# Optimization experiments

Measured on AMD Instinct MI355X. Metric: run time of the kernel, lower is better.

The kernel has to match this reference:

```python
import jax, jax.numpy as jnp
import numpy as np

B, C, N = 8, 128, 4096
C2 = C // 2
BN_EPS = 1e-5


def setup_inputs() -> dict:
    key = jax.random.key(0)
    ks = jax.random.split(key, 8)
    s = 1.0 / np.sqrt(C)
    s2 = 1.0 / np.sqrt(C2)
    return {
        "x": jax.random.normal(ks[0], (B, C, N), dtype=jnp.float32),
        "w_qk": jax.random.uniform(ks[1], (C2, C), jnp.float32, -s, s),  # shared q/k weight
        "w_v": jax.random.uniform(ks[2], (C2, C), jnp.float32, -s, s),
        "b_v": jax.random.uniform(ks[3], (C2,), jnp.float32, -s, s),
        "w_x": jax.random.uniform(ks[4], (C2, C), jnp.float32, -s, s),
        "w_t": jax.random.uniform(ks[5], (C2, C2), jnp.float32, -s2, s2),
        "b_t": jax.random.uniform(ks[6], (C2,), jnp.float32, -s2, s2),
        "gamma": jnp.ones((C2,), jnp.float32),
        "beta": jnp.zeros((C2,), jnp.float32),
    }


def reference(x, w_qk, w_v, b_v, w_x, w_t, b_t, gamma, beta):
    # 1x1 convs are per-point linear maps: [B,C,N] -> [B,C2,N]
    x_q = jnp.einsum("oc,bcn->bno", w_qk, x)          # [B, N, C2]
    x_k = jnp.einsum("oc,bcn->bon", w_qk, x)          # [B, C2, N]
    x_v = jnp.einsum("oc,bcn->bon", w_v, x) + b_v[None, :, None]

    energy = jnp.einsum("bno,bom->bnm", x_q, x_k)     # [B, N, N]
    attn = jax.nn.softmax(energy, axis=-1)            # row softmax
    attn = attn / (1e-9 + attn.sum(axis=1, keepdims=True))  # column L1 renorm

    x_r = jnp.einsum("bon,bnm->bom", x_v, attn)       # [B, C2, N]
    x_c = jnp.einsum("oc,bcn->bon", w_x, x)           # [B, C2, N]

    d = x_c - x_r
    t = jnp.einsum("oi,bin->bon", w_t, d) + b_t[None, :, None]
    # BatchNorm1d (training-mode batch stats) over (B, N) per channel
    mean = t.mean(axis=(0, 2), keepdims=True)
    var = t.var(axis=(0, 2), keepdims=True)
    t_hat = (t - mean) * jax.lax.rsqrt(var + BN_EPS)
    x_r2 = jax.nn.relu(gamma[None, :, None] * t_hat + beta[None, :, None])
    return x_c + x_r2
```

## Files before the change

### kernel.cpp

```cpp
#include <hip/hip_runtime.h>

#define B_   8
#define C_   128
#define N_   4096
#define C2_  64

typedef __bf16 bf16x8 __attribute__((ext_vector_type(8)));
typedef float  f32x4  __attribute__((ext_vector_type(4)));

#define MFMA16(a, b, c) __builtin_amdgcn_mfma_f32_16x16x32_bf16((a), (b), (c), 0, 0, 0)

#define QK_SCALE 1.2011224087864498f

static __device__ __forceinline__ unsigned short f2bf(float f) {
    union { __bf16 b; unsigned short u; } cv;
    cv.b = (__bf16)f;
    return cv.u;
}
static __device__ __forceinline__ float bf2f(unsigned short u) {
    union { unsigned int u; float f; } cv;
    cv.u = ((unsigned int)u) << 16;
    return cv.f;
}

struct us4 { unsigned short a, b, c, d; };

static __device__ __forceinline__ void gl_lds16(const unsigned short* g, void* l) {
    __builtin_amdgcn_global_load_lds(
        (const __attribute__((address_space(1))) unsigned int*)g,
        (__attribute__((address_space(3))) unsigned int*)l,
        16, 0, 0);
}

__global__ __launch_bounds__(256) void k1_proj(
    const float* __restrict__ x, const float* __restrict__ w_qk,
    const float* __restrict__ w_v, const float* __restrict__ b_v,
    const float* __restrict__ w_x,
    unsigned short* __restrict__ qk_t, unsigned short* __restrict__ xv_bf,
    float* __restrict__ xc)
{
    __shared__ __align__(16) unsigned short w_lds[192 * 136];
    __shared__ __align__(16) unsigned short x_t[64 * 136];
    const int tid = threadIdx.x;
    const int wave = tid >> 6, lane = tid & 63;
    const int quad = lane >> 4, col = lane & 15;
    const int b = blockIdx.y;
    const int n0 = blockIdx.x * 64;

    const float* wsrc[3] = {w_qk, w_v, w_x};
    #pragma unroll
    for (int mat = 0; mat < 3; ++mat) {
        const float* wm = wsrc[mat];
        #pragma unroll
        for (int it = 0; it < 8; ++it) {
            const int idx = it * 256 + tid;
            const int o = idx >> 5, c = (idx & 31) * 4;
            const float4 v = *(const float4*)(wm + o * C_ + c);
            us4 pk;
            pk.a = f2bf(v.x); pk.b = f2bf(v.y); pk.c = f2bf(v.z); pk.d = f2bf(v.w);
            *(us4*)&w_lds[(mat * 64 + o) * 136 + c] = pk;
        }
    }
    const float* xb = x + (size_t)b * C_ * N_ + n0;
    #pragma unroll
    for (int it = 0; it < 8; ++it) {
        const int idx = it * 256 + tid;
        const int c = idx >> 4, n = (idx & 15) * 4;
        const float4 v = *(const float4*)(xb + (size_t)c * N_ + n);
        x_t[(n + 0) * 136 + c] = f2bf(v.x);
        x_t[(n + 1) * 136 + c] = f2bf(v.y);
        x_t[(n + 2) * 136 + c] = f2bf(v.z);
        x_t[(n + 3) * 136 + c] = f2bf(v.w);
    }
    __syncthreads();

    const int nw = wave * 16;
    bf16x8 bfr[4];
    #pragma unroll
    for (int kt = 0; kt < 4; ++kt)
        bfr[kt] = *(const bf16x8*)&x_t[(nw + col) * 136 + kt * 32 + quad * 8];

    const int n_g = n0 + nw + col;

    #pragma unroll
    for (int ot = 0; ot < 12; ++ot) {
        f32x4 acc = {0.f, 0.f, 0.f, 0.f};
        #pragma unroll
        for (int kt = 0; kt < 4; ++kt) {
            const bf16x8 afr = *(const bf16x8*)&w_lds[(ot * 16 + col) * 136 + kt * 32 + quad * 8];
            acc = MFMA16(afr, bfr[kt], acc);
        }
        if (ot < 4) {
            us4 pk;
            pk.a = f2bf(acc[0] * QK_SCALE); pk.b = f2bf(acc[1] * QK_SCALE);
            pk.c = f2bf(acc[2] * QK_SCALE); pk.d = f2bf(acc[3] * QK_SCALE);
            *(us4*)&qk_t[(size_t)(b * N_ + n_g) * C2_ + ot * 16 + quad * 4] = pk;
        } else if (ot < 8) {
            const float4 bv4 = *(const float4*)(b_v + (ot - 4) * 16 + quad * 4);
            const float* bvp = (const float*)&bv4;
            #pragma unroll
            for (int r = 0; r < 4; ++r)
                xv_bf[(size_t)(b * C2_ + (ot - 4) * 16 + quad * 4 + r) * N_ + n_g]
                    = f2bf(acc[r] + bvp[r]);
        } else {
            #pragma unroll
            for (int r = 0; r < 4; ++r)
                xc[(size_t)(b * C2_ + (ot - 8) * 16 + quad * 4 + r) * N_ + n_g] = acc[r];
        }
    }
}

__global__ __launch_bounds__(256) void k2_rowstats(
    const unsigned short* __restrict__ qk_t, float* __restrict__ part_rs)
{
    __shared__ __align__(16) unsigned char lds_raw[2 * 16384];
    const int tid = threadIdx.x;
    const int wave = tid >> 6, lane = tid & 63;
    const int quad = lane >> 4, col = lane & 15;
    const int b = blockIdx.x & 7;
    const int nblk = (blockIdx.x >> 3) & 31;
    const int mq = blockIdx.x >> 8;
    const int n_base = nblk * 128 + wave * 32;
    const int m_start = mq * 512;
    const unsigned short* qb = qk_t + (size_t)b * N_ * C2_;

    bf16x8 a0[2], a1[2];
    #pragma unroll
    for (int s = 0; s < 2; ++s) {
        const unsigned short* p = qb + (size_t)(n_base + s * 16 + col) * C2_ + quad * 8;
        a0[s] = *(const bf16x8*)p;
        a1[s] = *(const bf16x8*)(p + 32);
    }

    auto stage = [&](int m0, int p) {
        unsigned char* base = lds_raw + p * 16384;
        #pragma unroll
        for (int r = 0; r < 4; ++r) {
            const int idx = r * 256 + tid;
            const int row = idx >> 3, seg = idx & 7;
            gl_lds16(qb + (size_t)(m0 + row) * C2_ + (size_t)(seg ^ (row & 7)) * 8,
                     base + idx * 16);
        }
    };

    float run_s[2][4];
    #pragma unroll
    for (int s = 0; s < 2; ++s)
        #pragma unroll
        for (int r = 0; r < 4; ++r) run_s[s][r] = 0.f;

    stage(m_start, 0);

    for (int c = 0; c < 4; ++c) {
        const int p = c & 1;
        asm volatile("s_waitcnt vmcnt(0)" ::: "memory");
        __builtin_amdgcn_s_barrier();
        asm volatile("" ::: "memory");
        if (c + 1 < 4) stage(m_start + (c + 1) * 128, 1 - p);
        const unsigned short* qt = (const unsigned short*)(lds_raw + p * 16384);
        #pragma unroll
        for (int ms = 0; ms < 8; ++ms) {
            const int row = ms * 16 + col;
            const bf16x8 b0 = *(const bf16x8*)(qt + row * 64 + ((quad ^ (col & 7)) * 8));
            const bf16x8 b1 = *(const bf16x8*)(qt + row * 64 + (((4 + quad) ^ (col & 7)) * 8));
            #pragma unroll
            for (int s = 0; s < 2; ++s) {
                f32x4 acc = {0.f, 0.f, 0.f, 0.f};
                __builtin_amdgcn_s_setprio(1);
                acc = MFMA16(a0[s], b0, acc);
                acc = MFMA16(a1[s], b1, acc);
                __builtin_amdgcn_s_setprio(0);
                #pragma unroll
                for (int r = 0; r < 4; ++r)
                    run_s[s][r] += __builtin_amdgcn_exp2f(acc[r]);
            }
        }
    }

    #pragma unroll
    for (int s = 0; s < 2; ++s)
        #pragma unroll
        for (int r = 0; r < 4; ++r) {
            #pragma unroll
            for (int off = 1; off < 16; off <<= 1)
                run_s[s][r] += __shfl_xor(run_s[s][r], off, 64);
        }
    if (col == 0) {
        #pragma unroll
        for (int s = 0; s < 2; ++s)
            #pragma unroll
            for (int r = 0; r < 4; ++r)
                part_rs[((size_t)(mq * 8 + b) << 12) + n_base + s * 16 + quad * 4 + r]
                    = run_s[s][r];
    }
}

__global__ __launch_bounds__(256) void k2bc(
    const float* __restrict__ part_rs, unsigned short* __restrict__ xv_bf,
    unsigned short* __restrict__ wbf)
{
    __shared__ float wl[64];
    const int tid = threadIdx.x;
    const int b = blockIdx.x & 7;
    const int n0 = (blockIdx.x >> 3) * 64;
    if (tid < 64) {
        float s = 0.f;
        #pragma unroll
        for (int q = 0; q < 8; ++q)
            s += part_rs[((size_t)(q * 8 + b) << 12) + n0 + tid];
        const float w = 1.0f / s;
        wl[tid] = w;
        wbf[b * N_ + n0 + tid] = f2bf(w);
    }
    __syncthreads();
    #pragma unroll
    for (int it = 0; it < 4; ++it) {
        const int idx4 = it * 256 + tid;
        const int o = idx4 >> 4, n4 = (idx4 & 15) * 4;
        unsigned short* p = xv_bf + (size_t)(b * C2_ + o) * N_ + n0 + n4;
        us4 v = *(us4*)p;
        v.a = f2bf(bf2f(v.a) * wl[n4 + 0]);
        v.b = f2bf(bf2f(v.b) * wl[n4 + 1]);
        v.c = f2bf(bf2f(v.c) * wl[n4 + 2]);
        v.d = f2bf(bf2f(v.d) * wl[n4 + 3]);
        *(us4*)p = v;
    }
}

__global__ __launch_bounds__(512, 4) void k3_pv(
    const unsigned short* __restrict__ qk_t, const unsigned short* __restrict__ xv_bf,
    const unsigned short* __restrict__ wbf,
    unsigned short* __restrict__ yb0, unsigned short* __restrict__ yb1,
    float* __restrict__ cspart)
{
    __shared__ __align__(16) unsigned char lds_raw[32768 + 8 * 2560];
    const int tid = threadIdx.x;
    const int wave = tid >> 6, lane = tid & 63;
    const int quad = lane >> 4, col = lane & 15;
    const int nh2 = wave & 1, mh = wave >> 1;
    const int b = blockIdx.x & 7;
    const int m_blk = ((blockIdx.x >> 3) & 31) * 128;
    const int sk = blockIdx.x >> 8;
    const int n_start = sk * 2048;
    const int n_chunks = 32;
    const int m_wave = m_blk + mh * 32;
    const unsigned short* qb = qk_t + (size_t)b * N_ * C2_;
    const unsigned short* vb = xv_bf + (size_t)b * C2_ * N_;
    const unsigned short* wb = wbf + b * N_;
    unsigned short* yp = (sk == 0) ? yb0 : yb1;

    bf16x8 kb0[2], kb1[2];
    #pragma unroll
    for (int g = 0; g < 2; ++g) {
        const unsigned short* p = qb + (size_t)(m_wave + g * 16 + col) * C2_ + quad * 8;
        kb0[g] = *(const bf16x8*)p;
        kb1[g] = *(const bf16x8*)(p + 32);
    }

    unsigned short* stS = (unsigned short*)(lds_raw + 32768 + wave * 2560);

    auto stage = [&](int n0, int p) {
        unsigned char* qbase = lds_raw + p * 8192;
        unsigned char* vbase = lds_raw + 16384 + p * 8192;
        const int row = tid >> 3, seg = tid & 7;
        const int ss = seg ^ (row & 7);
        gl_lds16(qb + (size_t)(n0 + row) * C2_ + (size_t)ss * 8, qbase + tid * 16);
        gl_lds16(vb + (size_t)row * N_ + n0 + ss * 8, vbase + tid * 16);
    };

    f32x4 accY[2][4];
    #pragma unroll
    for (int g = 0; g < 2; ++g)
        #pragma unroll
        for (int os = 0; os < 4; ++os) accY[g][os] = (f32x4){0.f, 0.f, 0.f, 0.f};
    f32x4 csacc[2];
    #pragma unroll
    for (int g = 0; g < 2; ++g) csacc[g] = (f32x4){0.f, 0.f, 0.f, 0.f};

    stage(n_start, 0);
    __syncthreads();

    for (int c = 0; c < n_chunks; ++c) {
        const int n0 = n_start + c * 64;
        const int p = c & 1;
        if (c + 1 < n_chunks) stage(n0 + 64, 1 - p);

        const unsigned short* qt = (const unsigned short*)(lds_raw + p * 8192);
        const unsigned short* vt = (const unsigned short*)(lds_raw + 16384 + p * 8192);

        const bf16x8 wfrag = *(const bf16x8*)(wb + n0 + nh2 * 32 + quad * 8);

        #pragma unroll
        for (int ns = 0; ns < 2; ++ns) {
            const int row = nh2 * 32 + ns * 16 + col;
            const bf16x8 qa0 = *(const bf16x8*)(qt + row * 64 + ((quad ^ (col & 7)) * 8));
            const bf16x8 qa1 = *(const bf16x8*)(qt + row * 64 + (((4 + quad) ^ (col & 7)) * 8));
            #pragma unroll
            for (int g = 0; g < 2; ++g) {
                f32x4 acc = {0.f, 0.f, 0.f, 0.f};
                acc = MFMA16(qa0, kb0[g], acc);
                acc = MFMA16(qa1, kb1[g], acc);
                union { unsigned short us[4]; uint2 u2; } pk;
                #pragma unroll
                for (int r = 0; r < 4; ++r)
                    pk.us[r] = f2bf(__builtin_amdgcn_exp2f(acc[r]));
                *(uint2*)&stS[(g * 16 + col) * 40 + ns * 16 + quad * 4] = pk.u2;
            }
        }

        bf16x8 sB[2];
        #pragma unroll
        for (int g = 0; g < 2; ++g)
            sB[g] = *(const bf16x8*)&stS[(g * 16 + col) * 40 + quad * 8];

        #pragma unroll
        for (int g = 0; g < 2; ++g)
            csacc[g] = MFMA16(wfrag, sB[g], csacc[g]);

        #pragma unroll
        for (int os = 0; os < 4; ++os) {
            const bf16x8 va = *(const bf16x8*)(vt + (os * 16 + col) * 64 +
                                               (((nh2 * 4 + quad) ^ (col & 7)) * 8));
            #pragma unroll
            for (int g = 0; g < 2; ++g)
                accY[g][os] = MFMA16(va, sB[g], accY[g][os]);
        }
        __syncthreads();
    }

    float* cmb = (float*)lds_raw;
    float* csc = (float*)(lds_raw + 32768);
    if (nh2 == 1) {
        #pragma unroll
        for (int g = 0; g < 2; ++g) {
            #pragma unroll
            for (int os = 0; os < 4; ++os)
                #pragma unroll
                for (int r = 0; r < 4; ++r)
                    cmb[((mh * 8 + g * 4 + os) * 4 + r) * 64 + lane] = accY[g][os][r];
            csc[(mh * 2 + g) * 64 + lane] = csacc[g][0];
        }
    }
    __syncthreads();
    if (nh2 == 0) {
        #pragma unroll
        for (int g = 0; g < 2; ++g) {
            const float cs = csacc[g][0] + csc[(mh * 2 + g) * 64 + lane];
            if (lane < 16)
                cspart[((size_t)sk * 8 + b) * N_ + m_wave + g * 16 + lane] = cs;
            #pragma unroll
            for (int os = 0; os < 4; ++os)
                #pragma unroll
                for (int r = 0; r < 4; ++r) {
                    const float v = accY[g][os][r] +
                        cmb[((mh * 8 + g * 4 + os) * 4 + r) * 64 + lane];
                    yp[(size_t)(b * C2_ + os * 16 + quad * 4 + r) * N_ + m_wave + g * 16 + col]
                        = f2bf(v);
                }
        }
    }
}

__global__ __launch_bounds__(256) void k4_t(
    const float* __restrict__ xc, const unsigned short* __restrict__ y0,
    const unsigned short* __restrict__ y1,
    const float* __restrict__ cspart, const float* __restrict__ w_t,
    const float* __restrict__ b_t, float* __restrict__ t_buf,
    float* __restrict__ part_bn)
{
    __shared__ __align__(16) unsigned short wlds[64 * 72];
    __shared__ __align__(16) unsigned short d_t[64 * 72];
    __shared__ float cinv[64];
    const int tid = threadIdx.x;
    const int wave = tid >> 6, lane = tid & 63;
    const int quad = lane >> 4, col = lane & 15;
    const int b = blockIdx.y;
    const int n0 = blockIdx.x * 64;
    const size_t base = (size_t)b * C2_ * N_;

    #pragma unroll
    for (int it = 0; it < 4; ++it) {
        const int idx4 = it * 256 + tid;
        const int o = idx4 >> 4, i4 = (idx4 & 15) * 4;
        const float4 v = *(const float4*)(w_t + o * 64 + i4);
        us4 pk;
        pk.a = f2bf(v.x); pk.b = f2bf(v.y); pk.c = f2bf(v.z); pk.d = f2bf(v.w);
        *(us4*)&wlds[o * 72 + i4] = pk;
    }
    if (tid < 64) {
        const int n = n0 + tid;
        const float cs = cspart[(size_t)b * N_ + n] + cspart[(size_t)(8 + b) * N_ + n];
        cinv[tid] = 1.0f / (1e-9f + cs);
    }
    __syncthreads();

    #pragma unroll
    for (int it = 0; it < 4; ++it) {
        const int idx4 = it * 256 + tid;
        const int i = idx4 >> 4, n4 = (idx4 & 15) * 4;
        const size_t g = base + (size_t)i * N_ + n0 + n4;
        const float4 c4 = *(const float4*)(xc + g);
        const us4 u0 = *(const us4*)(y0 + g);
        const us4 u1 = *(const us4*)(y1 + g);
        d_t[(n4 + 0) * 72 + i] = f2bf(c4.x - (bf2f(u0.a) + bf2f(u1.a)) * cinv[n4 + 0]);
        d_t[(n4 + 1) * 72 + i] = f2bf(c4.y - (bf2f(u0.b) + bf2f(u1.b)) * cinv[n4 + 1]);
        d_t[(n4 + 2) * 72 + i] = f2bf(c4.z - (bf2f(u0.c) + bf2f(u1.c)) * cinv[n4 + 2]);
        d_t[(n4 + 3) * 72 + i] = f2bf(c4.w - (bf2f(u0.d) + bf2f(u1.d)) * cinv[n4 + 3]);
    }
    __syncthreads();

    const int ow = wave * 16;
    bf16x8 afr[2];
    #pragma unroll
    for (int kt = 0; kt < 2; ++kt)
        afr[kt] = *(const bf16x8*)&wlds[(ow + col) * 72 + kt * 32 + quad * 8];
    const float4 bt4 = *(const float4*)(b_t + ow + quad * 4);
    const float* btp = (const float*)&bt4;

    float s[4] = {0.f, 0.f, 0.f, 0.f}, q2[4] = {0.f, 0.f, 0.f, 0.f};
    #pragma unroll
    for (int ns = 0; ns < 4; ++ns) {
        f32x4 acc = {0.f, 0.f, 0.f, 0.f};
        #pragma unroll
        for (int kt = 0; kt < 2; ++kt) {
            const bf16x8 bfr = *(const bf16x8*)&d_t[(ns * 16 + col) * 72 + kt * 32 + quad * 8];
            acc = MFMA16(afr[kt], bfr, acc);
        }
        #pragma unroll
        for (int r = 0; r < 4; ++r) {
            const float t = acc[r] + btp[r];
            t_buf[base + (size_t)(ow + quad * 4 + r) * N_ + n0 + ns * 16 + col] = t;
            s[r] += t;
            q2[r] += t * t;
        }
    }
    #pragma unroll
    for (int r = 0; r < 4; ++r) {
        #pragma unroll
        for (int off = 1; off < 16; off <<= 1) {
            s[r]  += __shfl_xor(s[r],  off, 64);
            q2[r] += __shfl_xor(q2[r], off, 64);
        }
    }
    if (col == 0) {
        const int blk = blockIdx.x * 8 + b;
        #pragma unroll
        for (int r = 0; r < 4; ++r) {
            part_bn[(size_t)(ow + quad * 4 + r) * 512 + blk]      = s[r];
            part_bn[(size_t)(64 + ow + quad * 4 + r) * 512 + blk] = q2[r];
        }
    }
}

__global__ __launch_bounds__(256) void k5r(
    const float* __restrict__ part_bn, float* __restrict__ bn)
{
    const int c = blockIdx.x;
    const int tid = threadIdx.x, wave = tid >> 6, lane = tid & 63;
    float s = 0.f;
    for (int j = tid; j < 512; j += 256) s += part_bn[(size_t)c * 512 + j];
    #pragma unroll
    for (int off = 1; off < 64; off <<= 1) s += __shfl_xor(s, off, 64);
    __shared__ float red[4];
    if (lane == 0) red[wave] = s;
    __syncthreads();
    if (tid == 0) bn[c] = red[0] + red[1] + red[2] + red[3];
}

__global__ __launch_bounds__(256) void k6_out(
    const float* __restrict__ xc, const float* __restrict__ t_buf,
    const float* __restrict__ bn, const float* __restrict__ gamma,
    const float* __restrict__ beta, float* __restrict__ out)
{
    const int idx = blockIdx.x * 256 + threadIdx.x;
    const int o = (idx >> 10) & 63;
    const float invC = 1.0f / (float)(B_ * N_);
    const float mean = bn[o] * invC;
    const float var  = bn[64 + o] * invC - mean * mean;
    const float sc = gamma[o] * rsqrtf(var + 1e-5f);
    const float sh = beta[o] - mean * sc;
    const float4 t4 = ((const float4*)t_buf)[idx];
    const float4 c4 = ((const float4*)xc)[idx];
    float4 r;
    r.x = c4.x + fmaxf(0.f, sc * t4.x + sh);
    r.y = c4.y + fmaxf(0.f, sc * t4.y + sh);
    r.z = c4.z + fmaxf(0.f, sc * t4.z + sh);
    r.w = c4.w + fmaxf(0.f, sc * t4.w + sh);
    ((float4*)out)[idx] = r;
}

extern "C" void kernel_launch(void* const* d_in, const int* in_sizes, int n_in,
                              void* d_out, int out_size, void* d_ws, size_t ws_size,
                              hipStream_t stream) {
    const float* x     = (const float*)d_in[0];
    const float* w_qk  = (const float*)d_in[1];
    const float* w_v   = (const float*)d_in[2];
    const float* b_v   = (const float*)d_in[3];
    const float* w_x   = (const float*)d_in[4];
    const float* w_t   = (const float*)d_in[5];
    const float* b_t   = (const float*)d_in[6];
    const float* gamma = (const float*)d_in[7];
    const float* beta  = (const float*)d_in[8];
    float* out = (float*)d_out;

    char* ws = (char*)d_ws;
    unsigned short* qk_t  = (unsigned short*)ws;
    unsigned short* xv_bf = (unsigned short*)(ws + (4  << 20));
    float* xc      = (float*)(ws + (8  << 20));
    unsigned short* yb0 = (unsigned short*)(ws + (16 << 20));
    unsigned short* yb1 = (unsigned short*)(ws + (20 << 20));
    float* t_buf   = (float*)(ws + (24 << 20));
    float* part_rs = (float*)(ws + (32 << 20));
    float* cspart  = (float*)(ws + (32 << 20));
    unsigned short* wbf = (unsigned short*)(ws + (33 << 20));
    float* part_bn = (float*)(ws + (33 << 20) + (64 << 10));
    float* bn      = (float*)(ws + (33 << 20) + (320 << 10));

    hipLaunchKernelGGL(k1_proj,     dim3(64, 8),  256, 0, stream,
                       x, w_qk, w_v, b_v, w_x, qk_t, xv_bf, xc);
    hipLaunchKernelGGL(k2_rowstats, dim3(2048),   256, 0, stream, qk_t, part_rs);
    hipLaunchKernelGGL(k2bc,        dim3(512),    256, 0, stream, part_rs, xv_bf, wbf);
    hipLaunchKernelGGL(k3_pv,       dim3(512),    512, 0, stream,
                       qk_t, xv_bf, wbf, yb0, yb1, cspart);
    hipLaunchKernelGGL(k4_t,        dim3(64, 8),  256, 0, stream,
                       xc, yb0, yb1, cspart, w_t, b_t, t_buf, part_bn);
    hipLaunchKernelGGL(k5r,         dim3(128),    256, 0, stream, part_bn, bn);
    hipLaunchKernelGGL(k6_out,      dim3(2048),   256, 0, stream, xc, t_buf, bn, gamma, beta, out);
}
```

Measured before the change: 165.1 us.

## Software-pipeline PV loop: compute exp(S) of next chunk while MMA-ing previous

Restructures the k3_pv main loop into a skewed software pipeline. The QK/exp phase for chunk c is issued before the PV and column-sum MFMAs for chunk c-1, and the S tiles are double-buffered in LDS. V fragments and weights are register-prefetched one iteration ahead. The aim is to overlap the exp/transcendental work with the MFMA work and drop a sync stall, at the cost of more LDS, more registers, and lowering launch_bounds occupancy from 4 to 3.

```diff
diff --git a/kernel.cpp b/kernel.cpp
--- a/kernel.cpp
+++ b/kernel.cpp
@@ -227,13 +227,13 @@
     }
 }
 
-__global__ __launch_bounds__(512, 4) void k3_pv(
+__global__ __launch_bounds__(512, 3) void k3_pv(
     const unsigned short* __restrict__ qk_t, const unsigned short* __restrict__ xv_bf,
     const unsigned short* __restrict__ wbf,
     unsigned short* __restrict__ yb0, unsigned short* __restrict__ yb1,
     float* __restrict__ cspart)
 {
-    __shared__ __align__(16) unsigned char lds_raw[32768 + 8 * 2560];
+    __shared__ __align__(16) unsigned char lds_raw[32768 + 8 * 5120];
     const int tid = threadIdx.x;
     const int wave = tid >> 6, lane = tid & 63;
     const int quad = lane >> 4, col = lane & 15;
@@ -257,7 +257,7 @@
         kb1[g] = *(const bf16x8*)(p + 32);
     }
 
-    unsigned short* stS = (unsigned short*)(lds_raw + 32768 + wave * 2560);
+    unsigned short* stSb = (unsigned short*)(lds_raw + 32768 + wave * 5120);
 
     auto stage = [&](int n0, int p) {
         unsigned char* qbase = lds_raw + p * 8192;
@@ -268,28 +268,9 @@
         gl_lds16(vb + (size_t)row * N_ + n0 + ss * 8, vbase + tid * 16);
     };
 
-    f32x4 accY[2][4];
-    #pragma unroll
-    for (int g = 0; g < 2; ++g)
-        #pragma unroll
-        for (int os = 0; os < 4; ++os) accY[g][os] = (f32x4){0.f, 0.f, 0.f, 0.f};
-    f32x4 csacc[2];
-    #pragma unroll
-    for (int g = 0; g < 2; ++g) csacc[g] = (f32x4){0.f, 0.f, 0.f, 0.f};
-
-    stage(n_start, 0);
-    __syncthreads();
-
-    for (int c = 0; c < n_chunks; ++c) {
-        const int n0 = n_start + c * 64;
-        const int p = c & 1;
-        if (c + 1 < n_chunks) stage(n0 + 64, 1 - p);
-
+    auto ephase = [&](int p) {
         const unsigned short* qt = (const unsigned short*)(lds_raw + p * 8192);
-        const unsigned short* vt = (const unsigned short*)(lds_raw + 16384 + p * 8192);
-
-        const bf16x8 wfrag = *(const bf16x8*)(wb + n0 + nh2 * 32 + quad * 8);
-
+        unsigned short* stW = stSb + p * 1280;
         #pragma unroll
         for (int ns = 0; ns < 2; ++ns) {
             const int row = nh2 * 32 + ns * 16 + col;
@@ -304,30 +285,90 @@
                 #pragma unroll
                 for (int r = 0; r < 4; ++r)
                     pk.us[r] = f2bf(__builtin_amdgcn_exp2f(acc[r]));
-                *(uint2*)&stS[(g * 16 + col) * 40 + ns * 16 + quad * 4] = pk.u2;
+                *(uint2*)&stW[(g * 16 + col) * 40 + ns * 16 + quad * 4] = pk.u2;
             }
         }
-
+    };
+
+    f32x4 accY[2][4];
+    #pragma unroll
+    for (int g = 0; g < 2; ++g)
+        #pragma unroll
+        for (int os = 0; os < 4; ++os) accY[g][os] = (f32x4){0.f, 0.f, 0.f, 0.f};
+    f32x4 csacc[2];
+    #pragma unroll
+    for (int g = 0; g < 2; ++g) csacc[g] = (f32x4){0.f, 0.f, 0.f, 0.f};
+
+    const int vsw = ((nh2 * 4 + quad) ^ (col & 7)) * 8;
+
+    stage(n_start, 0);
+    __syncthreads();
+    stage(n_start + 64, 1);
+
+    ephase(0);
+    bf16x8 vaP[4], wfP;
+    {
+        const unsigned short* vt = (const unsigned short*)(lds_raw + 16384);
+        #pragma unroll
+        for (int os = 0; os < 4; ++os)
+            vaP[os] = *(const bf16x8*)(vt + (os * 16 + col) * 64 + vsw);
+        wfP = *(const bf16x8*)(wb + n_start + nh2 * 32 + quad * 8);
+    }
+
+    for (int c = 1; c < n_chunks; ++c) {
+        const int n0 = n_start + c * 64;
+        const int p = c & 1;
+        __syncthreads();
+        if (c + 1 < n_chunks) stage(n0 + 64, 1 - p);
+
+        ephase(p);
+
+        bf16x8 vaC[4], wfC;
+        {
+            const unsigned short* vt = (const unsigned short*)(lds_raw + 16384 + p * 8192);
+            #pragma unroll
+            for (int os = 0; os < 4; ++os)
+                vaC[os] = *(const bf16x8*)(vt + (os * 16 + col) * 64 + vsw);
+            wfC = *(const bf16x8*)(wb + n0 + nh2 * 32 + quad * 8);
+        }
+
+        {
+            const unsigned short* stR = stSb + (1 - p) * 1280;
+            bf16x8 sB[2];
+            #pragma unroll
+            for (int g = 0; g < 2; ++g)
+                sB[g] = *(const bf16x8*)&stR[(g * 16 + col) * 40 + quad * 8];
+            #pragma unroll
+            for (int g = 0; g < 2; ++g)
+                csacc[g] = MFMA16(wfP, sB[g], csacc[g]);
+            #pragma unroll
+            for (int os = 0; os < 4; ++os)
+                #pragma unroll
+                for (int g = 0; g < 2; ++g)
+                    accY[g][os] = MFMA16(vaP[os], sB[g], accY[g][os]);
+        }
+        #pragma unroll
+        for (int os = 0; os < 4; ++os) vaP[os] = vaC[os];
+        wfP = wfC;
+    }
+
+    {
+        const unsigned short* stR = stSb + 1280;
         bf16x8 sB[2];
         #pragma unroll
         for (int g = 0; g < 2; ++g)
-            sB[g] = *(const bf16x8*)&stS[(g * 16 + col) * 40 + quad * 8];
-
+            sB[g] = *(const bf16x8*)&stR[(g * 16 + col) * 40 + quad * 8];
         #pragma unroll
         for (int g = 0; g < 2; ++g)
-            csacc[g] = MFMA16(wfrag, sB[g], csacc[g]);
-
-        #pragma unroll
-        for (int os = 0; os < 4; ++os) {
-            const bf16x8 va = *(const bf16x8*)(vt + (os * 16 + col) * 64 +
-                                               (((nh2 * 4 + quad) ^ (col & 7)) * 8));
+            csacc[g] = MFMA16(wfP, sB[g], csacc[g]);
+        #pragma unroll
+        for (int os = 0; os < 4; ++os)
             #pragma unroll
             for (int g = 0; g < 2; ++g)
-                accY[g][os] = MFMA16(va, sB[g], accY[g][os]);
-        }
-        __syncthreads();
-    }
-
+                accY[g][os] = MFMA16(vaP[os], sB[g], accY[g][os]);
+    }
+
+    __syncthreads();
     float* cmb = (float*)lds_raw;
     float* csc = (float*)(lds_raw + 32768);
     if (nh2 == 1) {
```

Result: slower. 170.3 us (+3.1%).

## Pre-convert weights once and fold row-sum normalisation into attention probabilities

Applied to the files above, without the earlier changes.

A new tiny kernel converts the three projection weights to bf16 once, folding the QK scale into the shared q/k weight. The projection kernel then loads them straight into a swizzled LDS layout with async global-to-LDS copies instead of converting in every block. The rescale pass over xv in k2bc is dropped: the per-row inverse sums are applied to the exponentials inside k3_pv, and the column-sum MFMA now uses an all-ones fragment. Staging buffers are placed in the output buffer as scratch, and k3 does a few more multiplies and loads per tile in exchange for one fewer full read/write pass over xv.

```diff
diff --git a/kernel.cpp b/kernel.cpp
--- a/kernel.cpp
+++ b/kernel.cpp
@@ -32,14 +32,28 @@
         16, 0, 0);
 }
 
+__global__ __launch_bounds__(256) void k0_wcvt(
+    const float* __restrict__ wq, const float* __restrict__ wv,
+    const float* __restrict__ wx, unsigned short* __restrict__ wst)
+{
+    const int i4 = (blockIdx.x * 256 + threadIdx.x) * 4;
+    const int mat = i4 >> 13;
+    const float* src = (mat == 0) ? wq : (mat == 1) ? wv : wx;
+    const float sc = (mat == 0) ? QK_SCALE : 1.0f;
+    const float4 v = *(const float4*)(src + (i4 & 8191));
+    us4 pk;
+    pk.a = f2bf(v.x * sc); pk.b = f2bf(v.y * sc);
+    pk.c = f2bf(v.z * sc); pk.d = f2bf(v.w * sc);
+    *(us4*)(wst + i4) = pk;
+}
+
 __global__ __launch_bounds__(256) void k1_proj(
-    const float* __restrict__ x, const float* __restrict__ w_qk,
-    const float* __restrict__ w_v, const float* __restrict__ b_v,
-    const float* __restrict__ w_x,
+    const float* __restrict__ x, const unsigned short* __restrict__ wst,
+    const float* __restrict__ b_v,
     unsigned short* __restrict__ qk_t, unsigned short* __restrict__ xv_bf,
     float* __restrict__ xc)
 {
-    __shared__ __align__(16) unsigned short w_lds[192 * 136];
+    __shared__ __align__(16) unsigned short w_lds[192 * 128];
     __shared__ __align__(16) unsigned short x_t[64 * 136];
     const int tid = threadIdx.x;
     const int wave = tid >> 6, lane = tid & 63;
@@ -47,19 +61,12 @@
     const int b = blockIdx.y;
     const int n0 = blockIdx.x * 64;
 
-    const float* wsrc[3] = {w_qk, w_v, w_x};
-    #pragma unroll
-    for (int mat = 0; mat < 3; ++mat) {
-        const float* wm = wsrc[mat];
-        #pragma unroll
-        for (int it = 0; it < 8; ++it) {
-            const int idx = it * 256 + tid;
-            const int o = idx >> 5, c = (idx & 31) * 4;
-            const float4 v = *(const float4*)(wm + o * C_ + c);
-            us4 pk;
-            pk.a = f2bf(v.x); pk.b = f2bf(v.y); pk.c = f2bf(v.z); pk.d = f2bf(v.w);
-            *(us4*)&w_lds[(mat * 64 + o) * 136 + c] = pk;
-        }
+    #pragma unroll
+    for (int it = 0; it < 12; ++it) {
+        const int idx = it * 256 + tid;
+        const int row = idx >> 4, seg = idx & 15;
+        gl_lds16(wst + (size_t)row * 128 + (size_t)(seg ^ (row & 7)) * 8,
+                 w_lds + idx * 8);
     }
     const float* xb = x + (size_t)b * C_ * N_ + n0;
     #pragma unroll
@@ -87,13 +94,14 @@
         f32x4 acc = {0.f, 0.f, 0.f, 0.f};
         #pragma unroll
         for (int kt = 0; kt < 4; ++kt) {
-            const bf16x8 afr = *(const bf16x8*)&w_lds[(ot * 16 + col) * 136 + kt * 32 + quad * 8];
+            const bf16x8 afr = *(const bf16x8*)&w_lds[
+                ((ot * 16 + col) << 7) + (((kt * 4 + quad) ^ (col & 7)) << 3)];
             acc = MFMA16(afr, bfr[kt], acc);
         }
         if (ot < 4) {
             us4 pk;
-            pk.a = f2bf(acc[0] * QK_SCALE); pk.b = f2bf(acc[1] * QK_SCALE);
-            pk.c = f2bf(acc[2] * QK_SCALE); pk.d = f2bf(acc[3] * QK_SCALE);
+            pk.a = f2bf(acc[0]); pk.b = f2bf(acc[1]);
+            pk.c = f2bf(acc[2]); pk.d = f2bf(acc[3]);
             *(us4*)&qk_t[(size_t)(b * N_ + n_g) * C2_ + ot * 16 + quad * 4] = pk;
         } else if (ot < 8) {
             const float4 bv4 = *(const float4*)(b_v + (ot - 4) * 16 + quad * 4);
@@ -195,41 +203,21 @@
     }
 }
 
-__global__ __launch_bounds__(256) void k2bc(
-    const float* __restrict__ part_rs, unsigned short* __restrict__ xv_bf,
-    unsigned short* __restrict__ wbf)
-{
-    __shared__ float wl[64];
-    const int tid = threadIdx.x;
+__global__ __launch_bounds__(64) void k2w(
+    const float* __restrict__ part_rs, float* __restrict__ winv)
+{
     const int b = blockIdx.x & 7;
-    const int n0 = (blockIdx.x >> 3) * 64;
-    if (tid < 64) {
-        float s = 0.f;
-        #pragma unroll
-        for (int q = 0; q < 8; ++q)
-            s += part_rs[((size_t)(q * 8 + b) << 12) + n0 + tid];
-        const float w = 1.0f / s;
-        wl[tid] = w;
-        wbf[b * N_ + n0 + tid] = f2bf(w);
-    }
-    __syncthreads();
-    #pragma unroll
-    for (int it = 0; it < 4; ++it) {
-        const int idx4 = it * 256 + tid;
-        const int o = idx4 >> 4, n4 = (idx4 & 15) * 4;
-        unsigned short* p = xv_bf + (size_t)(b * C2_ + o) * N_ + n0 + n4;
-        us4 v = *(us4*)p;
-        v.a = f2bf(bf2f(v.a) * wl[n4 + 0]);
-        v.b = f2bf(bf2f(v.b) * wl[n4 + 1]);
-        v.c = f2bf(bf2f(v.c) * wl[n4 + 2]);
-        v.d = f2bf(bf2f(v.d) * wl[n4 + 3]);
-        *(us4*)p = v;
-    }
+    const int n = (blockIdx.x >> 3) * 64 + threadIdx.x;
+    float s = 0.f;
+    #pragma unroll
+    for (int q = 0; q < 8; ++q)
+        s += part_rs[((size_t)(q * 8 + b) << 12) + n];
+    winv[b * N_ + n] = 1.0f / s;
 }
 
 __global__ __launch_bounds__(512, 4) void k3_pv(
     const unsigned short* __restrict__ qk_t, const unsigned short* __restrict__ xv_bf,
-    const unsigned short* __restrict__ wbf,
+    const float* __restrict__ winv,
     unsigned short* __restrict__ yb0, unsigned short* __restrict__ yb1,
     float* __restrict__ cspart)
 {
@@ -246,7 +234,7 @@
     const int m_wave = m_blk + mh * 32;
     const unsigned short* qb = qk_t + (size_t)b * N_ * C2_;
     const unsigned short* vb = xv_bf + (size_t)b * C2_ * N_;
-    const unsigned short* wb = wbf + b * N_;
+    const float* wn = winv + b * N_;
     unsigned short* yp = (sk == 0) ? yb0 : yb1;
 
     bf16x8 kb0[2], kb1[2];
@@ -256,6 +244,10 @@
         kb0[g] = *(const bf16x8*)p;
         kb1[g] = *(const bf16x8*)(p + 32);
     }
+
+    bf16x8 ones;
+    #pragma unroll
+    for (int j = 0; j < 8; ++j) ones[j] = (__bf16)1.0f;
 
     unsigned short* stS = (unsigned short*)(lds_raw + 32768 + wave * 2560);
 
@@ -288,13 +280,13 @@
         const unsigned short* qt = (const unsigned short*)(lds_raw + p * 8192);
         const unsigned short* vt = (const unsigned short*)(lds_raw + 16384 + p * 8192);
 
-        const bf16x8 wfrag = *(const bf16x8*)(wb + n0 + nh2 * 32 + quad * 8);
-
         #pragma unroll
         for (int ns = 0; ns < 2; ++ns) {
             const int row = nh2 * 32 + ns * 16 + col;
             const bf16x8 qa0 = *(const bf16x8*)(qt + row * 64 + ((quad ^ (col & 7)) * 8));
             const bf16x8 qa1 = *(const bf16x8*)(qt + row * 64 + (((4 + quad) ^ (col & 7)) * 8));
+            const float4 wv4 = *(const float4*)(wn + n0 + nh2 * 32 + ns * 16 + quad * 4);
+            const float* wv = (const float*)&wv4;
             #pragma unroll
             for (int g = 0; g < 2; ++g) {
                 f32x4 acc = {0.f, 0.f, 0.f, 0.f};
@@ -303,7 +295,7 @@
                 union { unsigned short us[4]; uint2 u2; } pk;
                 #pragma unroll
                 for (int r = 0; r < 4; ++r)
-                    pk.us[r] = f2bf(__builtin_amdgcn_exp2f(acc[r]));
+                    pk.us[r] = f2bf(wv[r] * __builtin_amdgcn_exp2f(acc[r]));
                 *(uint2*)&stS[(g * 16 + col) * 40 + ns * 16 + quad * 4] = pk.u2;
             }
         }
@@ -315,7 +307,7 @@
 
         #pragma unroll
         for (int g = 0; g < 2; ++g)
-            csacc[g] = MFMA16(wfrag, sB[g], csacc[g]);
+            csacc[g] = MFMA16(ones, sB[g], csacc[g]);
 
         #pragma unroll
         for (int os = 0; os < 4; ++os) {
@@ -512,16 +504,18 @@
     float* t_buf   = (float*)(ws + (24 << 20));
     float* part_rs = (float*)(ws + (32 << 20));
     float* cspart  = (float*)(ws + (32 << 20));
-    unsigned short* wbf = (unsigned short*)(ws + (33 << 20));
-    float* part_bn = (float*)(ws + (33 << 20) + (64 << 10));
-    float* bn      = (float*)(ws + (33 << 20) + (320 << 10));
-
+    float* part_bn = (float*)(ws + (33 << 20));
+    float* bn      = (float*)(ws + (33 << 20) + (256 << 10));
+    unsigned short* wstack = (unsigned short*)d_out;
+    float* winv = (float*)((char*)d_out + (256 << 10));
+
+    hipLaunchKernelGGL(k0_wcvt,     dim3(24),     256, 0, stream, w_qk, w_v, w_x, wstack);
     hipLaunchKernelGGL(k1_proj,     dim3(64, 8),  256, 0, stream,
-                       x, w_qk, w_v, b_v, w_x, qk_t, xv_bf, xc);
+                       x, wstack, b_v, qk_t, xv_bf, xc);
     hipLaunchKernelGGL(k2_rowstats, dim3(2048),   256, 0, stream, qk_t, part_rs);
-    hipLaunchKernelGGL(k2bc,        dim3(512),    256, 0, stream, part_rs, xv_bf, wbf);
+    hipLaunchKernelGGL(k2w,         dim3(512),    64,  0, stream, part_rs, winv);
     hipLaunchKernelGGL(k3_pv,       dim3(512),    512, 0, stream,
-                       qk_t, xv_bf, wbf, yb0, yb1, cspart);
+                       qk_t, xv_bf, winv, yb0, yb1, cspart);
     hipLaunchKernelGGL(k4_t,        dim3(64, 8),  256, 0, stream,
                        xc, yb0, yb1, cspart, w_t, b_t, t_buf, part_bn);
     hipLaunchKernelGGL(k5r,         dim3(128),    256, 0, stream, part_bn, bn);
```

Result: slower. 168.6 us (+2.1%).
